# Kernel optimization log

Measured on AMD Instinct MI355X. Metric: run time of the kernel, lower is better.

The kernel has to match this reference:

```python
import jax, jax.numpy as jnp
import numpy as np

NEG = -1e30  # log(0) surrogate that stays finite in fp32
BLANK = 0


def setup_inputs() -> dict:
    key = jax.random.key(0)
    k1, k2 = jax.random.split(key)
    B, T, V, L = 32, 1024, 1024, 256
    logits = jax.random.normal(k1, (B, T, V), dtype=jnp.float32)
    log_probs = jax.nn.log_softmax(logits, axis=-1)  # module expects log-probs
    labels = jax.random.randint(k2, (B, L), 1, V, dtype=jnp.int32)  # avoid blank=0
    input_lens = jnp.full((B,), T, dtype=jnp.int32)
    label_lens = jnp.full((B,), L, dtype=jnp.int32)
    return {"log_probs": log_probs, "labels": labels,
            "input_lens": input_lens, "label_lens": label_lens}


def _ctc_loss_sum(log_probs, labels, input_lens, label_lens, blank=BLANK):
    """CTC forward DP (alpha recursion) in log space; reduction='sum', zero_infinity=True."""
    B, T, V = log_probs.shape
    L = labels.shape[1]
    S = 2 * L + 1  # extended label: blank l1 blank l2 ... blank

    ext = jnp.full((B, S), blank, dtype=labels.dtype)
    ext = ext.at[:, 1::2].set(labels)
    # skip transition s-2 -> s allowed iff ext[s] != blank and ext[s] != ext[s-2]
    skip = jnp.concatenate(
        [jnp.zeros((B, 2), dtype=bool),
         (ext[:, 2:] != blank) & (ext[:, 2:] != ext[:, :-2])], axis=1)

    lp_tbv = jnp.transpose(log_probs, (1, 0, 2))  # 'btv->tbv' as in the module

    emit0 = jnp.take_along_axis(lp_tbv[0], ext, axis=1)  # [B,S]
    alpha0 = jnp.full((B, S), NEG, dtype=log_probs.dtype)
    alpha0 = alpha0.at[:, 0].set(emit0[:, 0]).at[:, 1].set(emit0[:, 1])

    neg1 = jnp.full((B, 1), NEG, dtype=log_probs.dtype)
    neg2 = jnp.full((B, 2), NEG, dtype=log_probs.dtype)

    def step(alpha, inputs):
        lp_t, t = inputs  # lp_t: [B,V]
        em = jnp.take_along_axis(lp_t, ext, axis=1)  # [B,S]
        a1 = alpha
        a2 = jnp.concatenate([neg1, alpha[:, :-1]], axis=1)
        a3 = jnp.where(skip, jnp.concatenate([neg2, alpha[:, :-2]], axis=1), NEG)
        new = jnp.logaddexp(jnp.logaddexp(a1, a2), a3) + em
        # freeze alpha once past this sample's input length
        new = jnp.where((t < input_lens)[:, None], new, alpha)
        return new, None

    ts = jnp.arange(1, T)
    alpha, _ = jax.lax.scan(step, alpha0, (lp_tbv[1:], ts))

    s_last = 2 * label_lens  # final blank state index per sample
    a_last = jnp.take_along_axis(alpha, s_last[:, None], axis=1)[:, 0]
    a_prev = jnp.take_along_axis(alpha, (s_last - 1)[:, None], axis=1)[:, 0]
    loss_b = -jnp.logaddexp(a_last, a_prev)
    loss_b = jnp.where(loss_b > 1e29, 0.0, loss_b)  # zero_infinity=True
    return jnp.sum(loss_b)


def reference(log_probs, labels, input_lens, label_lens):
    return _ctc_loss_sum(log_probs, labels, input_lens, label_lens)
```

## Files before the change

### kernel.cpp

```cpp
#include <hip/hip_runtime.h>


constexpr int B_ = 32, T_ = 1024, V_ = 1024, L_ = 256;
constexpr int S_ = 2 * L_ + 1;
constexpr int CH = 16;
constexpr int NCHUNK = 64;
constexpr int NBUF = 4;
constexpr float LN2F = 0.6931471805599453f;

typedef const __attribute__((address_space(1))) unsigned int* gp_t;
typedef __attribute__((address_space(3))) unsigned int* lp_t;

template <int CTRL>
__device__ __forceinline__ float dpp_fmax(float x) {
    const int t = __builtin_amdgcn_update_dpp(0, __float_as_int(x), CTRL, 0xf, 0xf, true);
    return fmaxf(x, __int_as_float(t));
}

__device__ __forceinline__ float wave_max_dpp(float x) {
    x = dpp_fmax<0x111>(x);
    x = dpp_fmax<0x112>(x);
    x = dpp_fmax<0x114>(x);
    x = dpp_fmax<0x118>(x);
    x = dpp_fmax<0x142>(x);
    x = dpp_fmax<0x143>(x);
    return __int_as_float(__builtin_amdgcn_readlane(__float_as_int(x), 63));
}

__device__ __forceinline__ float dpp_wave_shr1(float x) {
    return __int_as_float(
        __builtin_amdgcn_update_dpp(0, __float_as_int(x), 0x138, 0xf, 0xf, true));
}

__global__ __launch_bounds__(256, 4) void ctc_gather(
    float* __restrict__ lp, const int* __restrict__ labels,
    float* __restrict__ blanks)
{
    const int wave = threadIdx.x >> 6;
    const int lane = threadIdx.x & 63;
    const int r = blockIdx.x * 4 + wave;
    const int b = r >> 10;
    float* row = lp + (size_t)r * V_;
    const int* labb = labels + b * L_;

    const int4 e = *(const int4*)(labb + 4 * lane);
    const float v0 = row[e.x];
    const float v1 = row[e.y];
    const float v2 = row[e.z];
    const float v3 = row[e.w];
    const float vb = row[0];
    float4 q;
    q.x = __expf(v0); q.y = __expf(v1); q.z = __expf(v2); q.w = __expf(v3);
    const float qb = __expf(vb);
    __syncthreads();
    *(float4*)(row + 4 * lane) = q;
    if (lane == 0) {
        const int t = r & (T_ - 1);
        blanks[(r & ~(T_ - 1)) + ((t + T_ - 1) & (T_ - 1))] = qb;
    }
}

__global__ __launch_bounds__(128) void ctc_dp(
    const float* __restrict__ Q, const float* __restrict__ blanks,
    const int* __restrict__ labels, const int* __restrict__ input_lens,
    const int* __restrict__ label_lens, float* __restrict__ out)
{
    __shared__ float blk[T_ + 4];
    __shared__ float buf[NBUF][CH][256];
    __shared__ int Pf, Cf;
    const int b    = blockIdx.x;
    const int tid  = threadIdx.x;
    const int lane = tid & 63;
    const int wv   = tid >> 6;
    const float* Qb  = Q + (size_t)b * T_ * V_;
    const float* blg = blanks + b * T_;
    const int*  labb = labels + b * L_;
    const int il = input_lens[b];
    const int ll = label_lens[b];
    const int tend = il < T_ ? il : T_;

    if (tid == 0) { Pf = 0; Cf = 0; }
    __syncthreads();

    if (wv == 1) {
        #pragma unroll
        for (int i = 0; i < 4; ++i)
            __builtin_amdgcn_global_load_lds((gp_t)(blg + 256 * i + 4 * lane),
                                             (lp_t)&blk[256 * i], 16, 0, 0);
        #pragma unroll
        for (int i = 0; i < CH; ++i) {
            int t = 1 + i; if (t > T_ - 1) t = T_ - 1;
            __builtin_amdgcn_global_load_lds(
                (gp_t)(Qb + (size_t)t * V_ + 4 * lane),
                (lp_t)&buf[0][i][0], 16, 0, 0);
        }
        for (int c = 0; c < NCHUNK; ++c) {
            if (c + 1 < NCHUNK) {
                while (__hip_atomic_load(&Cf, __ATOMIC_ACQUIRE,
                                         __HIP_MEMORY_SCOPE_WORKGROUP) < c + 2 - NBUF) {}
                const int cb = (c + 1) & (NBUF - 1);
                #pragma unroll
                for (int i = 0; i < CH; ++i) {
                    int t = 1 + (c + 1) * CH + i; if (t > T_ - 1) t = T_ - 1;
                    __builtin_amdgcn_global_load_lds(
                        (gp_t)(Qb + (size_t)t * V_ + 4 * lane),
                        (lp_t)&buf[cb][i][0], 16, 0, 0);
                }
                asm volatile("s_waitcnt vmcnt(16)" ::: "memory");
            } else {
                asm volatile("s_waitcnt vmcnt(0)" ::: "memory");
            }
            if (lane == 0)
                __hip_atomic_store(&Pf, c + 1, __ATOMIC_RELEASE,
                                   __HIP_MEMORY_SCOPE_WORKGROUP);
        }
    } else {
        const int4 e  = *(const int4*)(labb + 4 * lane);
        const int  ep = (lane > 0) ? labb[4 * lane - 1] : -1;
        const float kf0 = ((8 * lane + 1) >= 3 && e.x != ep) ? 1.f : 0.f;
        const float kf1 = (e.y != e.x) ? 1.f : 0.f;
        const float kf2 = (e.z != e.y) ? 1.f : 0.f;
        const float kf3 = (e.w != e.z) ? 1.f : 0.f;
        const float bl0 = blg[T_ - 1];
        const float q00 = Qb[0];
        float p0 = (lane == 0) ? bl0 : 0.f;
        float p1 = (lane == 0) ? q00 : 0.f;
        float p2 = 0.f, p3 = 0.f, p4 = 0.f, p5 = 0.f,
              p6 = 0.f, p7 = 0.f, p8 = 0.f;
        int Esc = 0;
        float pm1 = 0.f;
        float sfP = 1.f, sfM = 1.f;

        auto snap = [&]() -> float {
            float m = fmaxf(fmaxf(fmaxf(fmaxf(p0, p1), fmaxf(p2, p3)),
                                  fmaxf(fmaxf(p4, p5), fmaxf(p6, p7))), p8);
            m = wave_max_dpp(m);
            const unsigned eb = (__float_as_uint(m) >> 23) & 0xffu;
            if (eb >= 1u && eb <= 254u) {
                unsigned k = 318u - eb;
                if (k > 254u) k = 254u;
                Esc += (int)k - 127;
                return __uint_as_float(k << 23);
            }
            return 1.f;
        };

        for (int c = 0; c < NCHUNK; ++c) {
            while (__hip_atomic_load(&Pf, __ATOMIC_ACQUIRE,
                                     __HIP_MEMORY_SCOPE_WORKGROUP) <= c) {}
            const float* base = &buf[c & (NBUF - 1)][0][0] + 4 * lane;
            float4 qA = *(const float4*)(base);
            float4 qB = *(const float4*)(base + 256);
            float4 qC = *(const float4*)(base + 512);
            float4 bv = *(const float4*)&blk[c * CH];
            float4 bvn;
            #pragma unroll
            for (int i = 0; i < CH; ++i) {
                const int g = i & 3;
                float qb = (g == 0) ? bv.x : (g == 1) ? bv.y
                         : (g == 2) ? bv.z : bv.w;
                float4 q = qA;
                qA = qB; qB = qC;
                if (i < CH - 3)
                    qC = *(const float4*)(base + (i + 3) * 256);
                if (g == 1) bvn = *(const float4*)&blk[c * CH + i + 3];
                if (g == 3) bv = bvn;
                if (i == 0) { q.x *= sfP; q.y *= sfP; q.z *= sfP; q.w *= sfP; qb *= sfP; }
                if (i == 8) { q.x *= sfM; q.y *= sfM; q.z *= sfM; q.w *= sfM; qb *= sfM; }
                const int t = 1 + c * CH + i;
                if (t < tend) {
                    const float n7 = fmaf(kf3, p5, p7 + p6) * q.w;
                    const float n8 = (p8 + p7) * qb;
                    const float pm1n = dpp_wave_shr1(n7);
                    const float n0 = (p0 + pm1) * qb;
                    const float n1 = fmaf(kf0, pm1, p1 + p0) * q.x;
                    const float n2 = (p2 + p1) * qb;
                    const float n3 = fmaf(kf1, p1, p3 + p2) * q.y;
                    const float n4 = (p4 + p3) * qb;
                    const float n5 = fmaf(kf2, p3, p5 + p4) * q.z;
                    const float n6 = (p6 + p5) * qb;
                    p0 = n0; p1 = n1; p2 = n2; p3 = n3; p4 = n4;
                    p5 = n5; p6 = n6; p7 = n7; p8 = n8; pm1 = pm1n;
                }
                if (i == 4)  sfM = snap();
                if (i == 12) sfP = snap();
            }
            if (lane == 0)
                __hip_atomic_store(&Cf, c + 1, __ATOMIC_RELEASE,
                                   __HIP_MEMORY_SCOPE_WORKGROUP);
        }
        p0 *= sfP; p1 *= sfP; p2 *= sfP; p3 *= sfP; p4 *= sfP;
        p5 *= sfP; p6 *= sfP; p7 *= sfP; p8 *= sfP;

        const int sl = 2 * ll;
        auto pick = [&](int s) -> float {
            if (s == 512) return __shfl(p8, 63);
            const int r = s & 7;
            float v = p0;
            v = (r == 1) ? p1 : v; v = (r == 2) ? p2 : v;
            v = (r == 3) ? p3 : v; v = (r == 4) ? p4 : v;
            v = (r == 5) ? p5 : v; v = (r == 6) ? p6 : v;
            v = (r == 7) ? p7 : v;
            return __shfl(v, s >> 3);
        };
        const float la = pick(sl);
        const float lb = pick(sl - 1);
        if (lane == 0) {
            const float tot = la + lb;
            float loss = (float)Esc * LN2F - __logf(tot);
            if (!(loss <= 1e29f)) loss = 0.f;
            atomicAdd(out, loss);
        }
    }
}

extern "C" void kernel_launch(void* const* d_in, const int* in_sizes, int n_in,
                              void* d_out, int out_size, void* d_ws, size_t ws_size,
                              hipStream_t stream) {
    float*       lp     = (float*)d_in[0];
    const int*   labels = (const int*)d_in[1];
    const int*   il     = (const int*)d_in[2];
    const int*   ll     = (const int*)d_in[3];
    float* out    = (float*)d_out;
    float* blanks = (float*)d_ws;

    hipMemsetAsync(out, 0, sizeof(float), stream);
    ctc_gather<<<dim3(B_ * T_ / 4), dim3(256), 0, stream>>>(lp, labels, blanks);
    ctc_dp<<<dim3(B_), dim3(128), 0, stream>>>(lp, blanks, labels, il, ll, out);
}
```

Measured before the change: 298.9 us.

## Stage gather rows into LDS via direct loads and batch DP chunk LDS reads

The gather kernel now copies each full log-prob row into shared memory with global_load_lds, then does the scattered label lookups from LDS instead of global memory. This removes the __syncthreads and raises the occupancy hint. The DP kernel now loads all 16 timesteps of a chunk into registers up front instead of software-pipelining three at a time, which trades higher register pressure for fewer LDS-latency stalls in the serial recurrence. The gather kernel reads the whole row where before it touched only the needed entries. Without the block barrier, the in-place row overwrite is only safe because each wave reads and writes its own row.

```diff
diff --git a/kernel.cpp b/kernel.cpp
--- a/kernel.cpp
+++ b/kernel.cpp
@@ -32,10 +32,11 @@
         __builtin_amdgcn_update_dpp(0, __float_as_int(x), 0x138, 0xf, 0xf, true));
 }
 
-__global__ __launch_bounds__(256, 4) void ctc_gather(
+__global__ __launch_bounds__(256, 8) void ctc_gather(
     float* __restrict__ lp, const int* __restrict__ labels,
     float* __restrict__ blanks)
 {
+    __shared__ float srow[4][V_];
     const int wave = threadIdx.x >> 6;
     const int lane = threadIdx.x & 63;
     const int r = blockIdx.x * 4 + wave;
@@ -43,16 +44,21 @@
     float* row = lp + (size_t)r * V_;
     const int* labb = labels + b * L_;
 
+    #pragma unroll
+    for (int j = 0; j < 4; ++j)
+        __builtin_amdgcn_global_load_lds((gp_t)(row + 256 * j + 4 * lane),
+                                         (lp_t)&srow[wave][256 * j], 16, 0, 0);
     const int4 e = *(const int4*)(labb + 4 * lane);
-    const float v0 = row[e.x];
-    const float v1 = row[e.y];
-    const float v2 = row[e.z];
-    const float v3 = row[e.w];
-    const float vb = row[0];
+    asm volatile("s_waitcnt vmcnt(0)" ::: "memory");
+    __builtin_amdgcn_sched_barrier(0);
+    const float v0 = srow[wave][e.x];
+    const float v1 = srow[wave][e.y];
+    const float v2 = srow[wave][e.z];
+    const float v3 = srow[wave][e.w];
+    const float vb = srow[wave][0];
     float4 q;
     q.x = __expf(v0); q.y = __expf(v1); q.z = __expf(v2); q.w = __expf(v3);
     const float qb = __expf(vb);
-    __syncthreads();
     *(float4*)(row + 4 * lane) = q;
     if (lane == 0) {
         const int t = r & (T_ - 1);
@@ -60,7 +66,7 @@
     }
 }
 
-__global__ __launch_bounds__(128) void ctc_dp(
+__global__ __launch_bounds__(128, 1) void ctc_dp(
     const float* __restrict__ Q, const float* __restrict__ blanks,
     const int* __restrict__ labels, const int* __restrict__ input_lens,
     const int* __restrict__ label_lens, float* __restrict__ out)
@@ -149,22 +155,21 @@
             while (__hip_atomic_load(&Pf, __ATOMIC_ACQUIRE,
                                      __HIP_MEMORY_SCOPE_WORKGROUP) <= c) {}
             const float* base = &buf[c & (NBUF - 1)][0][0] + 4 * lane;
-            float4 qA = *(const float4*)(base);
-            float4 qB = *(const float4*)(base + 256);
-            float4 qC = *(const float4*)(base + 512);
-            float4 bv = *(const float4*)&blk[c * CH];
-            float4 bvn;
+            float4 qv[CH];
+            #pragma unroll
+            for (int i = 0; i < CH; ++i)
+                qv[i] = *(const float4*)(base + 256 * i);
+            float bb[CH];
+            #pragma unroll
+            for (int i = 0; i < CH; i += 4) {
+                const float4 t4 = *(const float4*)&blk[c * CH + i];
+                bb[i] = t4.x; bb[i + 1] = t4.y;
+                bb[i + 2] = t4.z; bb[i + 3] = t4.w;
+            }
             #pragma unroll
             for (int i = 0; i < CH; ++i) {
-                const int g = i & 3;
-                float qb = (g == 0) ? bv.x : (g == 1) ? bv.y
-                         : (g == 2) ? bv.z : bv.w;
-                float4 q = qA;
-                qA = qB; qB = qC;
-                if (i < CH - 3)
-                    qC = *(const float4*)(base + (i + 3) * 256);
-                if (g == 1) bvn = *(const float4*)&blk[c * CH + i + 3];
-                if (g == 3) bv = bvn;
+                float4 q = qv[i];
+                float qb = bb[i];
                 if (i == 0) { q.x *= sfP; q.y *= sfP; q.z *= sfP; q.w *= sfP; qb *= sfP; }
                 if (i == 8) { q.x *= sfM; q.y *= sfM; q.z *= sfM; q.w *= sfM; qb *= sfM; }
                 const int t = 1 + c * CH + i;
```

Result: no change. 295.3 us (-1.2%).
